# Optimization experiments

Measured on AMD Instinct MI355X. Metric: run time of the kernel, lower is better.

Reference implementation:

```python
import jax, jax.numpy as jnp
import numpy as np

B, V, C, H, W, D = 2, 3, 8, 128, 160, 64


def bilinear_sample(feat, grid):
    """feat: [B,C,H,W]; grid: [B,N,2] normalized to [-1,1], align_corners=True,
    padding_mode='zeros' (matches F.grid_sample). Returns [B,C,N]."""
    b, c, h, w = feat.shape
    ix = (grid[..., 0] + 1.0) * 0.5 * (w - 1)  # [B,N]
    iy = (grid[..., 1] + 1.0) * 0.5 * (h - 1)
    x0 = jnp.floor(ix)
    y0 = jnp.floor(iy)
    wx1 = ix - x0
    wy1 = iy - y0
    flat = feat.reshape(b, c, h * w)

    def corner(xi, yi, wgt):
        valid = (xi >= 0) & (xi <= w - 1) & (yi >= 0) & (yi <= h - 1)
        xc = jnp.clip(xi, 0, w - 1).astype(jnp.int32)
        yc = jnp.clip(yi, 0, h - 1).astype(jnp.int32)
        idx = yc * w + xc  # [B,N]
        vals = jnp.take_along_axis(flat, jnp.broadcast_to(idx[:, None, :], (b, c, idx.shape[1])), axis=2)
        return vals * (wgt * valid.astype(feat.dtype))[:, None, :]

    out = (corner(x0, y0, (1 - wx1) * (1 - wy1))
           + corner(x0 + 1, y0, wx1 * (1 - wy1))
           + corner(x0, y0 + 1, (1 - wx1) * wy1)
           + corner(x0 + 1, y0 + 1, wx1 * wy1))
    return out


def homo_warping(src_feat, proj_mat, depth_values):
    """src_feat [B,C,H,W], proj_mat [B,3,4], depth_values [B,D,H,W].
    Returns warped volume [B,C,D,H,W] and normalized grid [B,D,H,W,2]."""
    b, c, h, w = src_feat.shape
    d = depth_values.shape[1]
    R = proj_mat[:, :, :3]
    T = proj_mat[:, :, 3:]  # [B,3,1]
    ys, xs = jnp.meshgrid(jnp.arange(h, dtype=src_feat.dtype),
                          jnp.arange(w, dtype=src_feat.dtype), indexing='ij')
    ref = jnp.stack([xs.ravel(), ys.ravel(), jnp.ones(h * w, src_feat.dtype)], 0)  # [3,HW]
    Rp = jnp.einsum('bij,jp->bip', R, ref)  # [B,3,HW]
    dv = depth_values.reshape(b, d, h * w)
    src = Rp[:, :, None, :] + T[:, :, :, None] / dv[:, None, :, :]  # [B,3,D,HW]
    xy = src[:, :2] / src[:, 2:3]
    gx = xy[:, 0] / ((w - 1) / 2.0) - 1.0
    gy = xy[:, 1] / ((h - 1) / 2.0) - 1.0
    grid = jnp.stack([gx, gy], axis=-1)  # [B,D,HW,2]
    warped = bilinear_sample(src_feat, grid.reshape(b, d * h * w, 2)).reshape(b, c, d, h, w)
    return warped, grid.reshape(b, d, h, w, 2)


def setup_inputs() -> dict:
    key = jax.random.key(0)
    k1, k2, k3, k4, k5 = jax.random.split(key, 5)
    features = jax.random.normal(k1, (V, B, C, H, W), dtype=jnp.float32)
    # near-identity projective maps so warps land mostly in-bounds
    eye = jnp.broadcast_to(jnp.eye(3, dtype=jnp.float32), (B, V, 3, 3))
    Rm = eye + 0.01 * jax.random.normal(k2, (B, V, 3, 3), dtype=jnp.float32)
    Tm = 2.0 * jax.random.normal(k3, (B, V, 3, 1), dtype=jnp.float32)
    proj_matrices = jnp.concatenate([Rm, Tm], axis=-1)  # [B,V,3,4]
    base = jnp.linspace(2.0, 10.0, D, dtype=jnp.float32)[None, :, None, None]
    depth_values = base + 0.1 * jax.random.uniform(k4, (B, D, H, W), dtype=jnp.float32)
    reg_weight = jax.random.normal(k5, (C,), dtype=jnp.float32)
    return {"features": features, "proj_matrices": proj_matrices,
            "depth_values": depth_values, "reg_weight": reg_weight,
            "num_depth": D}


def reference(features, proj_matrices, depth_values, reg_weight, num_depth):
    v = features.shape[0]
    ref_feat = features[0]
    b, c, h, w = ref_feat.shape
    d = num_depth
    ref_volume = jnp.broadcast_to(ref_feat[:, :, None], (b, c, d, h, w))
    volume_sum = ref_volume
    volume_sq_sum = ref_volume ** 2
    in_masks = jnp.ones((b, 1, d, h, w), dtype=ref_feat.dtype)
    for i in range(1, v):  # fixed small number of source views
        warped, grid = homo_warping(features[i], proj_matrices[:, i], depth_values)
        m = (grid > -1.0) & (grid < 1.0)
        in_masks = in_masks + (m[..., 0] & m[..., 1]).astype(ref_feat.dtype)[:, None]
        volume_sum = volume_sum + warped
        volume_sq_sum = volume_sq_sum + warped ** 2
    count = 1.0 / in_masks
    volume_feat = volume_sq_sum * count - (volume_sum * count) ** 2  # [B,C,D,H,W]
    # stand-in cost regularization: channel reduction -> [B,D,H,W]
    cost = jnp.einsum('bcdhw,c->bdhw', volume_feat, reg_weight)
    prob_volume = jax.nn.softmax(cost, axis=1)
    depth = jnp.sum(prob_volume * depth_values, axis=1)  # [B,H,W]
    return depth
```

## Files before the change

kernel.cpp:

```cpp
#include <hip/hip_runtime.h>
#include <math.h>

#define BB 2
#define VV 3
#define CC 8
#define HH 128
#define WW 160
#define DD 64
constexpr int HW = HH * WW;
constexpr int NPIX = BB * HW;
constexpr int PX_PER_BLOCK = 16;
constexpr int CHUNKS = 16;
constexpr int DEPTHS_PER_CHUNK = DD / CHUNKS;
constexpr int GRID_FUSED = NPIX / PX_PER_BLOCK;
constexpr int XCD_STRIDE = GRID_FUSED / 8;

typedef _Float16 h8 __attribute__((ext_vector_type(8)));

static __device__ __forceinline__ h8 splat8(float x) {
    const _Float16 v = (_Float16)x;
    h8 r = {v, v, v, v, v, v, v, v};
    return r;
}

__global__ __launch_bounds__(256)
void transpose_feats(const float* __restrict__ feats, h8* __restrict__ ft)
{
    const int t = blockIdx.x * blockDim.x + threadIdx.x;
    if (t >= VV * BB * HW) return;
    const int vb = t / HW;
    const int hw = t - vb * HW;
    const float* src = feats + (size_t)vb * CC * HW + hw;
    h8 v;
#pragma unroll
    for (int c = 0; c < CC; ++c) v[c] = (_Float16)src[(size_t)c * HW];
    ft[(size_t)vb * HW + hw] = v;
}

__global__ __launch_bounds__(256)
void transpose_dv(const float* __restrict__ dv, float* __restrict__ dvT)
{
    __shared__ float tile[64 * 65];
    const int t   = threadIdx.x;
    const int blk = blockIdx.x;
    const int b   = blk / (HW / 64);
    const int hw0 = (blk % (HW / 64)) * 64;

    const float* src = dv + (size_t)b * DD * HW + hw0;
    const int px = t & 63;
    const int dq = t >> 6;
#pragma unroll
    for (int j = 0; j < 16; ++j) {
        const int d = dq * 16 + j;
        tile[px * 65 + d] = src[(size_t)d * HW + px];
    }
    __syncthreads();

    float* dst = dvT + ((size_t)b * HW + hw0) * DD;
    const int c = t & 15;
#pragma unroll
    for (int j = 0; j < 4; ++j) {
        const int p = (t >> 4) + j * 16;
        float4 v;
        v.x = tile[p * 65 + c * 4 + 0];
        v.y = tile[p * 65 + c * 4 + 1];
        v.z = tile[p * 65 + c * 4 + 2];
        v.w = tile[p * 65 + c * 4 + 3];
        ((float4*)(dst + (size_t)p * DD))[c] = v;
    }
}

__global__ __launch_bounds__(256)
void depthnet_fused(const h8* __restrict__ ft,
                    const float* __restrict__ proj,
                    const float* __restrict__ dvT,
                    const float* __restrict__ regw,
                    float* __restrict__ out)
{
    __shared__ float sm_m[4 * PX_PER_BLOCK];
    __shared__ float sm_l[4 * PX_PER_BLOCK];
    __shared__ float sm_s[4 * PX_PER_BLOCK];

    const int tid   = threadIdx.x;
    const int lane  = tid & 63;
    const int wave  = tid >> 6;
    const int px    = lane & 15;
    const int sub   = lane >> 4;
    const int chunk = wave * 4 + sub;
    const int bswz  = (blockIdx.x & 7) * XCD_STRIDE + (blockIdx.x >> 3);
    const int pixel = bswz * PX_PER_BLOCK + px;

    const int b  = (pixel >= HW) ? 1 : 0;
    const int hw = pixel - b * HW;
    const int h  = hw / WW;
    const int w  = hw - h * WW;

    float rf[CC], rf2[CC];
    {
        h8 rv = ft[(size_t)b * HW + hw];
#pragma unroll
        for (int c = 0; c < CC; ++c) { rf[c] = (float)rv[c]; rf2[c] = rf[c] * rf[c]; }
    }

    float Rp[2][3], Tv[2][3];
    const float xf = (float)w, yf = (float)h;
#pragma unroll
    for (int v = 0; v < 2; ++v) {
        const float* M = proj + ((size_t)b * VV + (v + 1)) * 12;
#pragma unroll
        for (int i = 0; i < 3; ++i) {
            Rp[v][i] = M[i * 4 + 0] * xf + M[i * 4 + 1] * yf + M[i * 4 + 2];
            Tv[v][i] = M[i * 4 + 3];
        }
    }

    const h8* fsrc0 = ft + (size_t)(1 * BB + b) * HW;
    const h8* fsrc1 = ft + (size_t)(2 * BB + b) * HW;

    const float4 dv4 = *(const float4*)(dvT + ((size_t)b * HW + hw) * DD + chunk * 4);
    float dvv[4] = {dv4.x, dv4.y, dv4.z, dv4.w};
    float inv[4];
#pragma unroll
    for (int k = 0; k < 4; ++k) inv[k] = __builtin_amdgcn_rcpf(dvv[k]);

    float m = -INFINITY, l = 0.f, s = 0.f;

    for (int dd = 0; dd < DEPTHS_PER_CHUNK; ++dd) {
        const float dv = dvv[dd];
        const float inv_dv = inv[dd];

        float wt[2][4];
        int   ib[2][4];
        float nmask = 1.0f;
#pragma unroll
        for (int v = 0; v < 2; ++v) {
            const float sx = Rp[v][0] + Tv[v][0] * inv_dv;
            const float sy = Rp[v][1] + Tv[v][1] * inv_dv;
            const float sz = Rp[v][2] + Tv[v][2] * inv_dv;
            const float rsz = __builtin_amdgcn_rcpf(sz);
            const float ix = sx * rsz;
            const float iy = sy * rsz;
            nmask += ((ix > 0.f) && (ix < (float)(WW - 1)) &&
                      (iy > 0.f) && (iy < (float)(HH - 1))) ? 1.0f : 0.0f;
            const float x0f = floorf(ix), y0f = floorf(iy);
            const float wx1 = ix - x0f, wy1 = iy - y0f;
            const float wx0 = 1.f - wx1, wy0 = 1.f - wy1;
            const float x1f = x0f + 1.f, y1f = y0f + 1.f;
            const bool vx0 = (x0f >= 0.f) && (x0f <= (float)(WW - 1));
            const bool vx1 = (x1f >= 0.f) && (x1f <= (float)(WW - 1));
            const bool vy0 = (y0f >= 0.f) && (y0f <= (float)(HH - 1));
            const bool vy1 = (y1f >= 0.f) && (y1f <= (float)(HH - 1));
            wt[v][0] = wx0 * wy0 * ((vx0 && vy0) ? 1.f : 0.f);
            wt[v][1] = wx1 * wy0 * ((vx1 && vy0) ? 1.f : 0.f);
            wt[v][2] = wx0 * wy1 * ((vx0 && vy1) ? 1.f : 0.f);
            wt[v][3] = wx1 * wy1 * ((vx1 && vy1) ? 1.f : 0.f);
            const int x0c = (int)fminf(fmaxf(x0f, 0.f), (float)(WW - 1));
            const int x1c = (int)fminf(fmaxf(x1f, 0.f), (float)(WW - 1));
            const int y0c = (int)fminf(fmaxf(y0f, 0.f), (float)(HH - 1));
            const int y1c = (int)fminf(fmaxf(y1f, 0.f), (float)(HH - 1));
            ib[v][0] = y0c * WW + x0c;
            ib[v][1] = y0c * WW + x1c;
            ib[v][2] = y1c * WW + x0c;
            ib[v][3] = y1c * WW + x1c;
        }

        h8 a0 = fsrc0[ib[0][0]];
        h8 a1 = fsrc0[ib[0][1]];
        h8 a2 = fsrc0[ib[0][2]];
        h8 a3 = fsrc0[ib[0][3]];
        h8 b0 = fsrc1[ib[1][0]];
        h8 b1 = fsrc1[ib[1][1]];
        h8 b2 = fsrc1[ib[1][2]];
        h8 b3 = fsrc1[ib[1][3]];

        h8 vah = a0 * splat8(wt[0][0]) + a1 * splat8(wt[0][1])
               + a2 * splat8(wt[0][2]) + a3 * splat8(wt[0][3]);
        h8 vbh = b0 * splat8(wt[1][0]) + b1 * splat8(wt[1][1])
               + b2 * splat8(wt[1][2]) + b3 * splat8(wt[1][3]);

        float sum[CC], sq[CC];
#pragma unroll
        for (int c = 0; c < CC; ++c) {
            const float av = (float)vah[c];
            const float bv = (float)vbh[c];
            sum[c] = rf[c] + av + bv;
            sq[c]  = rf2[c] + av * av + bv * bv;
        }

        const float cnt = __builtin_amdgcn_rcpf(nmask);
        float t1 = 0.f, t2 = 0.f;
#pragma unroll
        for (int c = 0; c < CC; ++c) {
            t1 += regw[c] * sq[c];
            t2 += (regw[c] * sum[c]) * sum[c];
        }
        const float cost = cnt * t1 - (cnt * cnt) * t2;

        const float M = fmaxf(m, cost);
        const float e_old = __expf(m - M);
        const float e_new = __expf(cost - M);
        l = l * e_old + e_new;
        s = s * e_old + e_new * dv;
        m = M;
    }

#pragma unroll
    for (int off = 16; off < 64; off <<= 1) {
        const float m2 = __shfl_xor(m, off, 64);
        const float l2 = __shfl_xor(l, off, 64);
        const float s2 = __shfl_xor(s, off, 64);
        const float M  = fmaxf(m, m2);
        const float e1 = __expf(m - M);
        const float e2 = __expf(m2 - M);
        l = l * e1 + l2 * e2;
        s = s * e1 + s2 * e2;
        m = M;
    }

    if (lane < PX_PER_BLOCK) {
        sm_m[wave * PX_PER_BLOCK + px] = m;
        sm_l[wave * PX_PER_BLOCK + px] = l;
        sm_s[wave * PX_PER_BLOCK + px] = s;
    }
    __syncthreads();

    if (tid < PX_PER_BLOCK) {
        float M = sm_m[tid], L = sm_l[tid], S = sm_s[tid];
#pragma unroll
        for (int wv = 1; wv < 4; ++wv) {
            const float m2 = sm_m[wv * PX_PER_BLOCK + tid];
            const float l2 = sm_l[wv * PX_PER_BLOCK + tid];
            const float s2 = sm_s[wv * PX_PER_BLOCK + tid];
            const float Mn = fmaxf(M, m2);
            const float e1 = __expf(M - Mn);
            const float e2 = __expf(m2 - Mn);
            L = L * e1 + l2 * e2;
            S = S * e1 + s2 * e2;
            M = Mn;
        }
        out[bswz * PX_PER_BLOCK + tid] = S / L;
    }
}

extern "C" void kernel_launch(void* const* d_in, const int* in_sizes, int n_in,
                              void* d_out, int out_size, void* d_ws, size_t ws_size,
                              hipStream_t stream) {
    const float* feats  = (const float*)d_in[0];
    const float* proj   = (const float*)d_in[1];
    const float* depthv = (const float*)d_in[2];
    const float* regw   = (const float*)d_in[3];
    float* out = (float*)d_out;
    h8*    ft  = (h8*)d_ws;
    float* dvT = (float*)d_ws + (size_t)VV * BB * HW * CC / 2;

    {
        const int n = VV * BB * HW;
        hipLaunchKernelGGL(transpose_feats, dim3((n + 255) / 256), dim3(256), 0, stream,
                           feats, ft);
    }
    {
        const int grid = BB * (HW / 64);
        hipLaunchKernelGGL(transpose_dv, dim3(grid), dim3(256), 0, stream,
                           depthv, dvT);
    }
    {
        hipLaunchKernelGGL(depthnet_fused, dim3(GRID_FUSED), dim3(256), 0, stream,
                           ft, proj, dvT, regw, out);
    }
}
```

Before: 103.0 us.

## Split fused kernel into per-depth cost kernel and separate softmax pass

Replaces the depth-transpose plus fused per-pixel loop with two kernels. One thread per (pixel, depth) computes the cost and writes it to a workspace volume. A second kernel runs an online softmax over depth with coalesced reads. This removes the depth-transpose kernel and the serial per-thread depth loop, and gives more parallelism. The cost is an extra round trip of the full cost volume (B*D*HW floats) through memory and a re-read of the depth values.

```diff
diff --git a/kernel.cpp b/kernel.cpp
--- a/kernel.cpp
+++ b/kernel.cpp
@@ -9,11 +9,8 @@
 #define DD 64
 constexpr int HW = HH * WW;
 constexpr int NPIX = BB * HW;
-constexpr int PX_PER_BLOCK = 16;
-constexpr int CHUNKS = 16;
-constexpr int DEPTHS_PER_CHUNK = DD / CHUNKS;
-constexpr int GRID_FUSED = NPIX / PX_PER_BLOCK;
-constexpr int XCD_STRIDE = GRID_FUSED / 8;
+constexpr int PIXBANDS = NPIX / 256;
+constexpr int BANDS_PER_XCD = PIXBANDS / 8;
 
 typedef _Float16 h8 __attribute__((ext_vector_type(8)));
 
@@ -38,57 +35,18 @@
 }
 
 __global__ __launch_bounds__(256)
-void transpose_dv(const float* __restrict__ dv, float* __restrict__ dvT)
+void cost_kernel(const h8* __restrict__ ft,
+                 const float* __restrict__ proj,
+                 const float* __restrict__ depthv,
+                 const float* __restrict__ regw,
+                 float* __restrict__ cost_out)
 {
-    __shared__ float tile[64 * 65];
-    const int t   = threadIdx.x;
-    const int blk = blockIdx.x;
-    const int b   = blk / (HW / 64);
-    const int hw0 = (blk % (HW / 64)) * 64;
-
-    const float* src = dv + (size_t)b * DD * HW + hw0;
-    const int px = t & 63;
-    const int dq = t >> 6;
-#pragma unroll
-    for (int j = 0; j < 16; ++j) {
-        const int d = dq * 16 + j;
-        tile[px * 65 + d] = src[(size_t)d * HW + px];
-    }
-    __syncthreads();
-
-    float* dst = dvT + ((size_t)b * HW + hw0) * DD;
-    const int c = t & 15;
-#pragma unroll
-    for (int j = 0; j < 4; ++j) {
-        const int p = (t >> 4) + j * 16;
-        float4 v;
-        v.x = tile[p * 65 + c * 4 + 0];
-        v.y = tile[p * 65 + c * 4 + 1];
-        v.z = tile[p * 65 + c * 4 + 2];
-        v.w = tile[p * 65 + c * 4 + 3];
-        ((float4*)(dst + (size_t)p * DD))[c] = v;
-    }
-}
-
-__global__ __launch_bounds__(256)
-void depthnet_fused(const h8* __restrict__ ft,
-                    const float* __restrict__ proj,
-                    const float* __restrict__ dvT,
-                    const float* __restrict__ regw,
-                    float* __restrict__ out)
-{
-    __shared__ float sm_m[4 * PX_PER_BLOCK];
-    __shared__ float sm_l[4 * PX_PER_BLOCK];
-    __shared__ float sm_s[4 * PX_PER_BLOCK];
-
-    const int tid   = threadIdx.x;
-    const int lane  = tid & 63;
-    const int wave  = tid >> 6;
-    const int px    = lane & 15;
-    const int sub   = lane >> 4;
-    const int chunk = wave * 4 + sub;
-    const int bswz  = (blockIdx.x & 7) * XCD_STRIDE + (blockIdx.x >> 3);
-    const int pixel = bswz * PX_PER_BLOCK + px;
+    const int i    = blockIdx.x;
+    const int xcd  = i & 7;
+    const int idx  = i >> 3;
+    const int band = xcd * BANDS_PER_XCD + (idx % BANDS_PER_XCD);
+    const int d    = idx / BANDS_PER_XCD;
+    const int pixel = band * 256 + threadIdx.x;
 
     const int b  = (pixel >= HW) ? 1 : 0;
     const int hw = pixel - b * HW;
@@ -108,97 +66,110 @@
     for (int v = 0; v < 2; ++v) {
         const float* M = proj + ((size_t)b * VV + (v + 1)) * 12;
 #pragma unroll
-        for (int i = 0; i < 3; ++i) {
-            Rp[v][i] = M[i * 4 + 0] * xf + M[i * 4 + 1] * yf + M[i * 4 + 2];
-            Tv[v][i] = M[i * 4 + 3];
+        for (int j = 0; j < 3; ++j) {
+            Rp[v][j] = M[j * 4 + 0] * xf + M[j * 4 + 1] * yf + M[j * 4 + 2];
+            Tv[v][j] = M[j * 4 + 3];
         }
     }
 
     const h8* fsrc0 = ft + (size_t)(1 * BB + b) * HW;
     const h8* fsrc1 = ft + (size_t)(2 * BB + b) * HW;
 
-    const float4 dv4 = *(const float4*)(dvT + ((size_t)b * HW + hw) * DD + chunk * 4);
-    float dvv[4] = {dv4.x, dv4.y, dv4.z, dv4.w};
-    float inv[4];
-#pragma unroll
-    for (int k = 0; k < 4; ++k) inv[k] = __builtin_amdgcn_rcpf(dvv[k]);
+    const float dv = depthv[(size_t)b * DD * HW + (size_t)d * HW + hw];
+    const float inv_dv = __builtin_amdgcn_rcpf(dv);
+
+    float wt[2][4];
+    int   ib[2][4];
+    float nmask = 1.0f;
+#pragma unroll
+    for (int v = 0; v < 2; ++v) {
+        const float sx = Rp[v][0] + Tv[v][0] * inv_dv;
+        const float sy = Rp[v][1] + Tv[v][1] * inv_dv;
+        const float sz = Rp[v][2] + Tv[v][2] * inv_dv;
+        const float rsz = __builtin_amdgcn_rcpf(sz);
+        const float ix = sx * rsz;
+        const float iy = sy * rsz;
+        nmask += ((ix > 0.f) && (ix < (float)(WW - 1)) &&
+                  (iy > 0.f) && (iy < (float)(HH - 1))) ? 1.0f : 0.0f;
+        const float x0f = floorf(ix), y0f = floorf(iy);
+        const float wx1 = ix - x0f, wy1 = iy - y0f;
+        const float wx0 = 1.f - wx1, wy0 = 1.f - wy1;
+        const float x1f = x0f + 1.f, y1f = y0f + 1.f;
+        const bool vx0 = (x0f >= 0.f) && (x0f <= (float)(WW - 1));
+        const bool vx1 = (x1f >= 0.f) && (x1f <= (float)(WW - 1));
+        const bool vy0 = (y0f >= 0.f) && (y0f <= (float)(HH - 1));
+        const bool vy1 = (y1f >= 0.f) && (y1f <= (float)(HH - 1));
+        wt[v][0] = wx0 * wy0 * ((vx0 && vy0) ? 1.f : 0.f);
+        wt[v][1] = wx1 * wy0 * ((vx1 && vy0) ? 1.f : 0.f);
+        wt[v][2] = wx0 * wy1 * ((vx0 && vy1) ? 1.f : 0.f);
+        wt[v][3] = wx1 * wy1 * ((vx1 && vy1) ? 1.f : 0.f);
+        const int x0c = (int)fminf(fmaxf(x0f, 0.f), (float)(WW - 1));
+        const int x1c = (int)fminf(fmaxf(x1f, 0.f), (float)(WW - 1));
+        const int y0c = (int)fminf(fmaxf(y0f, 0.f), (float)(HH - 1));
+        const int y1c = (int)fminf(fmaxf(y1f, 0.f), (float)(HH - 1));
+        ib[v][0] = y0c * WW + x0c;
+        ib[v][1] = y0c * WW + x1c;
+        ib[v][2] = y1c * WW + x0c;
+        ib[v][3] = y1c * WW + x1c;
+    }
+
+    h8 a0 = fsrc0[ib[0][0]];
+    h8 a1 = fsrc0[ib[0][1]];
+    h8 a2 = fsrc0[ib[0][2]];
+    h8 a3 = fsrc0[ib[0][3]];
+    h8 b0 = fsrc1[ib[1][0]];
+    h8 b1 = fsrc1[ib[1][1]];
+    h8 b2 = fsrc1[ib[1][2]];
+    h8 b3 = fsrc1[ib[1][3]];
+
+    h8 vah = a0 * splat8(wt[0][0]) + a1 * splat8(wt[0][1])
+           + a2 * splat8(wt[0][2]) + a3 * splat8(wt[0][3]);
+    h8 vbh = b0 * splat8(wt[1][0]) + b1 * splat8(wt[1][1])
+           + b2 * splat8(wt[1][2]) + b3 * splat8(wt[1][3]);
+
+    const float cnt = __builtin_amdgcn_rcpf(nmask);
+    float t1 = 0.f, t2 = 0.f;
+#pragma unroll
+    for (int c = 0; c < CC; ++c) {
+        const float av = (float)vah[c];
+        const float bv = (float)vbh[c];
+        const float sum = rf[c] + av + bv;
+        const float sq  = rf2[c] + av * av + bv * bv;
+        t1 += regw[c] * sq;
+        t2 += (regw[c] * sum) * sum;
+    }
+    const float cost = cnt * t1 - (cnt * cnt) * t2;
+
+    cost_out[(size_t)b * DD * HW + (size_t)d * HW + hw] = cost;
+}
+
+__global__ __launch_bounds__(256)
+void softmax_depth(const float* __restrict__ cost,
+                   const float* __restrict__ depthv,
+                   float* __restrict__ out)
+{
+    const int t     = blockIdx.x * blockDim.x + threadIdx.x;
+    const int lane  = t & 63;
+    const int waveg = t >> 6;
+    const int px    = lane & 15;
+    const int chunk = lane >> 4;
+    const int pixel = waveg * 16 + px;
+
+    const int b  = (pixel >= HW) ? 1 : 0;
+    const int hw = pixel - b * HW;
+
+    const float* cp = cost   + (size_t)b * DD * HW + hw;
+    const float* dp = depthv + (size_t)b * DD * HW + hw;
 
     float m = -INFINITY, l = 0.f, s = 0.f;
-
-    for (int dd = 0; dd < DEPTHS_PER_CHUNK; ++dd) {
-        const float dv = dvv[dd];
-        const float inv_dv = inv[dd];
-
-        float wt[2][4];
-        int   ib[2][4];
-        float nmask = 1.0f;
-#pragma unroll
-        for (int v = 0; v < 2; ++v) {
-            const float sx = Rp[v][0] + Tv[v][0] * inv_dv;
-            const float sy = Rp[v][1] + Tv[v][1] * inv_dv;
-            const float sz = Rp[v][2] + Tv[v][2] * inv_dv;
-            const float rsz = __builtin_amdgcn_rcpf(sz);
-            const float ix = sx * rsz;
-            const float iy = sy * rsz;
-            nmask += ((ix > 0.f) && (ix < (float)(WW - 1)) &&
-                      (iy > 0.f) && (iy < (float)(HH - 1))) ? 1.0f : 0.0f;
-            const float x0f = floorf(ix), y0f = floorf(iy);
-            const float wx1 = ix - x0f, wy1 = iy - y0f;
-            const float wx0 = 1.f - wx1, wy0 = 1.f - wy1;
-            const float x1f = x0f + 1.f, y1f = y0f + 1.f;
-            const bool vx0 = (x0f >= 0.f) && (x0f <= (float)(WW - 1));
-            const bool vx1 = (x1f >= 0.f) && (x1f <= (float)(WW - 1));
-            const bool vy0 = (y0f >= 0.f) && (y0f <= (float)(HH - 1));
-            const bool vy1 = (y1f >= 0.f) && (y1f <= (float)(HH - 1));
-            wt[v][0] = wx0 * wy0 * ((vx0 && vy0) ? 1.f : 0.f);
-            wt[v][1] = wx1 * wy0 * ((vx1 && vy0) ? 1.f : 0.f);
-            wt[v][2] = wx0 * wy1 * ((vx0 && vy1) ? 1.f : 0.f);
-            wt[v][3] = wx1 * wy1 * ((vx1 && vy1) ? 1.f : 0.f);
-            const int x0c = (int)fminf(fmaxf(x0f, 0.f), (float)(WW - 1));
-            const int x1c = (int)fminf(fmaxf(x1f, 0.f), (float)(WW - 1));
-            const int y0c = (int)fminf(fmaxf(y0f, 0.f), (float)(HH - 1));
-            const int y1c = (int)fminf(fmaxf(y1f, 0.f), (float)(HH - 1));
-            ib[v][0] = y0c * WW + x0c;
-            ib[v][1] = y0c * WW + x1c;
-            ib[v][2] = y1c * WW + x0c;
-            ib[v][3] = y1c * WW + x1c;
-        }
-
-        h8 a0 = fsrc0[ib[0][0]];
-        h8 a1 = fsrc0[ib[0][1]];
-        h8 a2 = fsrc0[ib[0][2]];
-        h8 a3 = fsrc0[ib[0][3]];
-        h8 b0 = fsrc1[ib[1][0]];
-        h8 b1 = fsrc1[ib[1][1]];
-        h8 b2 = fsrc1[ib[1][2]];
-        h8 b3 = fsrc1[ib[1][3]];
-
-        h8 vah = a0 * splat8(wt[0][0]) + a1 * splat8(wt[0][1])
-               + a2 * splat8(wt[0][2]) + a3 * splat8(wt[0][3]);
-        h8 vbh = b0 * splat8(wt[1][0]) + b1 * splat8(wt[1][1])
-               + b2 * splat8(wt[1][2]) + b3 * splat8(wt[1][3]);
-
-        float sum[CC], sq[CC];
-#pragma unroll
-        for (int c = 0; c < CC; ++c) {
-            const float av = (float)vah[c];
-            const float bv = (float)vbh[c];
-            sum[c] = rf[c] + av + bv;
-            sq[c]  = rf2[c] + av * av + bv * bv;
-        }
-
-        const float cnt = __builtin_amdgcn_rcpf(nmask);
-        float t1 = 0.f, t2 = 0.f;
-#pragma unroll
-        for (int c = 0; c < CC; ++c) {
-            t1 += regw[c] * sq[c];
-            t2 += (regw[c] * sum[c]) * sum[c];
-        }
-        const float cost = cnt * t1 - (cnt * cnt) * t2;
-
-        const float M = fmaxf(m, cost);
+#pragma unroll 4
+    for (int j = 0; j < 16; ++j) {
+        const int d = chunk * 16 + j;
+        const float c  = cp[(size_t)d * HW];
+        const float dv = dp[(size_t)d * HW];
+        const float M = fmaxf(m, c);
         const float e_old = __expf(m - M);
-        const float e_new = __expf(cost - M);
+        const float e_new = __expf(c - M);
         l = l * e_old + e_new;
         s = s * e_old + e_new * dv;
         m = M;
@@ -217,29 +188,7 @@
         m = M;
     }
 
-    if (lane < PX_PER_BLOCK) {
-        sm_m[wave * PX_PER_BLOCK + px] = m;
-        sm_l[wave * PX_PER_BLOCK + px] = l;
-        sm_s[wave * PX_PER_BLOCK + px] = s;
-    }
-    __syncthreads();
-
-    if (tid < PX_PER_BLOCK) {
-        float M = sm_m[tid], L = sm_l[tid], S = sm_s[tid];
-#pragma unroll
-        for (int wv = 1; wv < 4; ++wv) {
-            const float m2 = sm_m[wv * PX_PER_BLOCK + tid];
-            const float l2 = sm_l[wv * PX_PER_BLOCK + tid];
-            const float s2 = sm_s[wv * PX_PER_BLOCK + tid];
-            const float Mn = fmaxf(M, m2);
-            const float e1 = __expf(M - Mn);
-            const float e2 = __expf(m2 - Mn);
-            L = L * e1 + l2 * e2;
-            S = S * e1 + s2 * e2;
-            M = Mn;
-        }
-        out[bswz * PX_PER_BLOCK + tid] = S / L;
-    }
+    if (chunk == 0) out[pixel] = s / l;
 }
 
 extern "C" void kernel_launch(void* const* d_in, const int* in_sizes, int n_in,
@@ -250,8 +199,8 @@
     const float* depthv = (const float*)d_in[2];
     const float* regw   = (const float*)d_in[3];
     float* out = (float*)d_out;
-    h8*    ft  = (h8*)d_ws;
-    float* dvT = (float*)d_ws + (size_t)VV * BB * HW * CC / 2;
+    h8*    ft   = (h8*)d_ws;
+    float* cost = (float*)((char*)d_ws + (size_t)VV * BB * HW * sizeof(h8));
 
     {
         const int n = VV * BB * HW;
@@ -259,12 +208,13 @@
                            feats, ft);
     }
     {
-        const int grid = BB * (HW / 64);
-        hipLaunchKernelGGL(transpose_dv, dim3(grid), dim3(256), 0, stream,
-                           depthv, dvT);
-    }
-    {
-        hipLaunchKernelGGL(depthnet_fused, dim3(GRID_FUSED), dim3(256), 0, stream,
-                           ft, proj, dvT, regw, out);
-    }
-}
+        const int grid = DD * PIXBANDS;
+        hipLaunchKernelGGL(cost_kernel, dim3(grid), dim3(256), 0, stream,
+                           ft, proj, depthv, regw, cost);
+    }
+    {
+        const int total = NPIX * 4;
+        hipLaunchKernelGGL(softmax_depth, dim3(total / 256), dim3(256), 0, stream,
+                           cost, depthv, out);
+    }
+}
```

Measured after the change: 103.0 us. No clear change (-0.1%).

## Drop depth transpose kernel, read depths directly, and reuse bilinear gathers across depths

Applied to the files above, without the earlier changes.

Removes the separate depth-value transpose kernel and reads depth values straight from the original layout inside the fused kernel. Consecutive lanes map to consecutive pixels, so these reads stay coalesced. The block now covers 32 pixels with 8 depth chunks of 8 depths each, and the XCD swizzle is dropped. Projection is computed as R·p·d + T, which avoids the per-depth reciprocal. The fused kernel also skips re-gathering corner features when the bilinear indices match the previous depth, and uses a two-pass softmax per chunk instead of an online update. This saves a launch and a workspace round trip, at the cost of more registers and more divergent branches around the gathers.

```diff
diff --git a/kernel.cpp b/kernel.cpp
--- a/kernel.cpp
+++ b/kernel.cpp
@@ -9,11 +9,9 @@
 #define DD 64
 constexpr int HW = HH * WW;
 constexpr int NPIX = BB * HW;
-constexpr int PX_PER_BLOCK = 16;
-constexpr int CHUNKS = 16;
-constexpr int DEPTHS_PER_CHUNK = DD / CHUNKS;
-constexpr int GRID_FUSED = NPIX / PX_PER_BLOCK;
-constexpr int XCD_STRIDE = GRID_FUSED / 8;
+constexpr int PX_PER_BLOCK = 32;
+constexpr int CHUNKS = 8;
+constexpr int DPC = DD / CHUNKS;
 
 typedef _Float16 h8 __attribute__((ext_vector_type(8)));
 
@@ -38,42 +36,9 @@
 }
 
 __global__ __launch_bounds__(256)
-void transpose_dv(const float* __restrict__ dv, float* __restrict__ dvT)
-{
-    __shared__ float tile[64 * 65];
-    const int t   = threadIdx.x;
-    const int blk = blockIdx.x;
-    const int b   = blk / (HW / 64);
-    const int hw0 = (blk % (HW / 64)) * 64;
-
-    const float* src = dv + (size_t)b * DD * HW + hw0;
-    const int px = t & 63;
-    const int dq = t >> 6;
-#pragma unroll
-    for (int j = 0; j < 16; ++j) {
-        const int d = dq * 16 + j;
-        tile[px * 65 + d] = src[(size_t)d * HW + px];
-    }
-    __syncthreads();
-
-    float* dst = dvT + ((size_t)b * HW + hw0) * DD;
-    const int c = t & 15;
-#pragma unroll
-    for (int j = 0; j < 4; ++j) {
-        const int p = (t >> 4) + j * 16;
-        float4 v;
-        v.x = tile[p * 65 + c * 4 + 0];
-        v.y = tile[p * 65 + c * 4 + 1];
-        v.z = tile[p * 65 + c * 4 + 2];
-        v.w = tile[p * 65 + c * 4 + 3];
-        ((float4*)(dst + (size_t)p * DD))[c] = v;
-    }
-}
-
-__global__ __launch_bounds__(256)
 void depthnet_fused(const h8* __restrict__ ft,
                     const float* __restrict__ proj,
-                    const float* __restrict__ dvT,
+                    const float* __restrict__ depthv,
                     const float* __restrict__ regw,
                     float* __restrict__ out)
 {
@@ -84,11 +49,10 @@
     const int tid   = threadIdx.x;
     const int lane  = tid & 63;
     const int wave  = tid >> 6;
-    const int px    = lane & 15;
-    const int sub   = lane >> 4;
-    const int chunk = wave * 4 + sub;
-    const int bswz  = (blockIdx.x & 7) * XCD_STRIDE + (blockIdx.x >> 3);
-    const int pixel = bswz * PX_PER_BLOCK + px;
+    const int px    = lane & 31;
+    const int sub   = lane >> 5;
+    const int chunk = wave * 2 + sub;
+    const int pixel = blockIdx.x * PX_PER_BLOCK + px;
 
     const int b  = (pixel >= HW) ? 1 : 0;
     const int hw = pixel - b * HW;
@@ -108,35 +72,36 @@
     for (int v = 0; v < 2; ++v) {
         const float* M = proj + ((size_t)b * VV + (v + 1)) * 12;
 #pragma unroll
-        for (int i = 0; i < 3; ++i) {
-            Rp[v][i] = M[i * 4 + 0] * xf + M[i * 4 + 1] * yf + M[i * 4 + 2];
-            Tv[v][i] = M[i * 4 + 3];
+        for (int j = 0; j < 3; ++j) {
+            Rp[v][j] = M[j * 4 + 0] * xf + M[j * 4 + 1] * yf + M[j * 4 + 2];
+            Tv[v][j] = M[j * 4 + 3];
         }
     }
 
     const h8* fsrc0 = ft + (size_t)(1 * BB + b) * HW;
     const h8* fsrc1 = ft + (size_t)(2 * BB + b) * HW;
 
-    const float4 dv4 = *(const float4*)(dvT + ((size_t)b * HW + hw) * DD + chunk * 4);
-    float dvv[4] = {dv4.x, dv4.y, dv4.z, dv4.w};
-    float inv[4];
-#pragma unroll
-    for (int k = 0; k < 4; ++k) inv[k] = __builtin_amdgcn_rcpf(dvv[k]);
-
-    float m = -INFINITY, l = 0.f, s = 0.f;
-
-    for (int dd = 0; dd < DEPTHS_PER_CHUNK; ++dd) {
-        const float dv = dvv[dd];
-        const float inv_dv = inv[dd];
+    const float* dvp = depthv + (size_t)b * DD * HW + hw;
+    float dvv[DPC];
+#pragma unroll
+    for (int k = 0; k < DPC; ++k) dvv[k] = dvp[(size_t)(chunk * DPC + k) * HW];
+
+    float cost[DPC];
+    h8 A0, A1, A2, A3, B0, B1, B2, B3;
+    int pa0 = 0, pa3 = 0, pb0 = 0, pb3 = 0;
+
+#pragma unroll
+    for (int k = 0; k < DPC; ++k) {
+        const float d = dvv[k];
 
         float wt[2][4];
         int   ib[2][4];
         float nmask = 1.0f;
 #pragma unroll
         for (int v = 0; v < 2; ++v) {
-            const float sx = Rp[v][0] + Tv[v][0] * inv_dv;
-            const float sy = Rp[v][1] + Tv[v][1] * inv_dv;
-            const float sz = Rp[v][2] + Tv[v][2] * inv_dv;
+            const float sx = Rp[v][0] * d + Tv[v][0];
+            const float sy = Rp[v][1] * d + Tv[v][1];
+            const float sz = Rp[v][2] * d + Tv[v][2];
             const float rsz = __builtin_amdgcn_rcpf(sz);
             const float ix = sx * rsz;
             const float iy = sy * rsz;
@@ -164,51 +129,58 @@
             ib[v][3] = y1c * WW + x1c;
         }
 
-        h8 a0 = fsrc0[ib[0][0]];
-        h8 a1 = fsrc0[ib[0][1]];
-        h8 a2 = fsrc0[ib[0][2]];
-        h8 a3 = fsrc0[ib[0][3]];
-        h8 b0 = fsrc1[ib[1][0]];
-        h8 b1 = fsrc1[ib[1][1]];
-        h8 b2 = fsrc1[ib[1][2]];
-        h8 b3 = fsrc1[ib[1][3]];
-
-        h8 vah = a0 * splat8(wt[0][0]) + a1 * splat8(wt[0][1])
-               + a2 * splat8(wt[0][2]) + a3 * splat8(wt[0][3]);
-        h8 vbh = b0 * splat8(wt[1][0]) + b1 * splat8(wt[1][1])
-               + b2 * splat8(wt[1][2]) + b3 * splat8(wt[1][3]);
-
-        float sum[CC], sq[CC];
+        if (k == 0) {
+            A0 = fsrc0[ib[0][0]]; A1 = fsrc0[ib[0][1]];
+            A2 = fsrc0[ib[0][2]]; A3 = fsrc0[ib[0][3]];
+            B0 = fsrc1[ib[1][0]]; B1 = fsrc1[ib[1][1]];
+            B2 = fsrc1[ib[1][2]]; B3 = fsrc1[ib[1][3]];
+        } else {
+            if (ib[0][0] != pa0 || ib[0][3] != pa3) {
+                A0 = fsrc0[ib[0][0]]; A1 = fsrc0[ib[0][1]];
+                A2 = fsrc0[ib[0][2]]; A3 = fsrc0[ib[0][3]];
+            }
+            if (ib[1][0] != pb0 || ib[1][3] != pb3) {
+                B0 = fsrc1[ib[1][0]]; B1 = fsrc1[ib[1][1]];
+                B2 = fsrc1[ib[1][2]]; B3 = fsrc1[ib[1][3]];
+            }
+        }
+        pa0 = ib[0][0]; pa3 = ib[0][3];
+        pb0 = ib[1][0]; pb3 = ib[1][3];
+
+        h8 vah = A0 * splat8(wt[0][0]) + A1 * splat8(wt[0][1])
+               + A2 * splat8(wt[0][2]) + A3 * splat8(wt[0][3]);
+        h8 vbh = B0 * splat8(wt[1][0]) + B1 * splat8(wt[1][1])
+               + B2 * splat8(wt[1][2]) + B3 * splat8(wt[1][3]);
+
+        const float cnt = __builtin_amdgcn_rcpf(nmask);
+        float t1 = 0.f, t2 = 0.f;
 #pragma unroll
         for (int c = 0; c < CC; ++c) {
             const float av = (float)vah[c];
             const float bv = (float)vbh[c];
-            sum[c] = rf[c] + av + bv;
-            sq[c]  = rf2[c] + av * av + bv * bv;
-        }
-
-        const float cnt = __builtin_amdgcn_rcpf(nmask);
-        float t1 = 0.f, t2 = 0.f;
-#pragma unroll
-        for (int c = 0; c < CC; ++c) {
-            t1 += regw[c] * sq[c];
-            t2 += (regw[c] * sum[c]) * sum[c];
-        }
-        const float cost = cnt * t1 - (cnt * cnt) * t2;
-
-        const float M = fmaxf(m, cost);
-        const float e_old = __expf(m - M);
-        const float e_new = __expf(cost - M);
-        l = l * e_old + e_new;
-        s = s * e_old + e_new * dv;
-        m = M;
-    }
-
-#pragma unroll
-    for (int off = 16; off < 64; off <<= 1) {
-        const float m2 = __shfl_xor(m, off, 64);
-        const float l2 = __shfl_xor(l, off, 64);
-        const float s2 = __shfl_xor(s, off, 64);
+            const float sum = rf[c] + av + bv;
+            const float sq  = rf2[c] + av * av + bv * bv;
+            t1 += regw[c] * sq;
+            t2 += (regw[c] * sum) * sum;
+        }
+        cost[k] = cnt * t1 - (cnt * cnt) * t2;
+    }
+
+    float m = cost[0];
+#pragma unroll
+    for (int k = 1; k < DPC; ++k) m = fmaxf(m, cost[k]);
+    float l = 0.f, s = 0.f;
+#pragma unroll
+    for (int k = 0; k < DPC; ++k) {
+        const float e = __expf(cost[k] - m);
+        l += e;
+        s += e * dvv[k];
+    }
+
+    {
+        const float m2 = __shfl_xor(m, 32, 64);
+        const float l2 = __shfl_xor(l, 32, 64);
+        const float s2 = __shfl_xor(s, 32, 64);
         const float M  = fmaxf(m, m2);
         const float e1 = __expf(m - M);
         const float e2 = __expf(m2 - M);
@@ -238,7 +210,7 @@
             S = S * e1 + s2 * e2;
             M = Mn;
         }
-        out[bswz * PX_PER_BLOCK + tid] = S / L;
+        out[blockIdx.x * PX_PER_BLOCK + tid] = S / L;
     }
 }
 
@@ -250,8 +222,7 @@
     const float* depthv = (const float*)d_in[2];
     const float* regw   = (const float*)d_in[3];
     float* out = (float*)d_out;
-    h8*    ft  = (h8*)d_ws;
-    float* dvT = (float*)d_ws + (size_t)VV * BB * HW * CC / 2;
+    h8* ft = (h8*)d_ws;
 
     {
         const int n = VV * BB * HW;
@@ -259,12 +230,8 @@
                            feats, ft);
     }
     {
-        const int grid = BB * (HW / 64);
-        hipLaunchKernelGGL(transpose_dv, dim3(grid), dim3(256), 0, stream,
-                           depthv, dvT);
-    }
-    {
-        hipLaunchKernelGGL(depthnet_fused, dim3(GRID_FUSED), dim3(256), 0, stream,
-                           ft, proj, dvT, regw, out);
-    }
-}
+        const int grid = NPIX / PX_PER_BLOCK;
+        hipLaunchKernelGGL(depthnet_fused, dim3(grid), dim3(256), 0, stream,
+                           ft, proj, depthv, regw, out);
+    }
+}
```

After: 108.7 us. 5.5% more time.
